# Kernel tuning notes

Measured on AMD Instinct MI355X. Metric: run time of the kernel, lower is better.

The kernel has to match this reference:

```python
import jax, jax.numpy as jnp
import numpy as np

V, E, H0, H1 = 32000, 512, 1024, 1024
B, S = 32, 128


def setup_inputs() -> dict:
    key = jax.random.key(0)
    ks = jax.random.split(key, 10)
    s = 0.02
    tokens = jax.random.randint(ks[0], (B, S), 0, V)
    emb = jax.random.normal(ks[1], (V, E), dtype=jnp.float32) * s
    W0 = jax.random.normal(ks[2], (E, H0), dtype=jnp.float32) * s
    U0 = jax.random.normal(ks[3], (H0, H0), dtype=jnp.float32) * s
    b0 = jnp.zeros((H0,), dtype=jnp.float32)
    W1 = jax.random.normal(ks[4], (H0, H1), dtype=jnp.float32) * s
    U1 = jax.random.normal(ks[5], (H1, H1), dtype=jnp.float32) * s
    b1 = jnp.zeros((H1,), dtype=jnp.float32)
    Wd = jax.random.normal(ks[6], (H1, V), dtype=jnp.float32) * s
    bd = jnp.zeros((V,), dtype=jnp.float32)
    return {"tokens": tokens, "emb": emb, "W0": W0, "U0": U0, "b0": b0,
            "W1": W1, "U1": U1, "b1": b1, "Wd": Wd, "bd": bd}


def reference(tokens, emb, W0, U0, b0, W1, U1, b1, Wd, bd):
    # Embedding lookup: [B, S, E]
    x = emb[tokens]
    # Stacked SimpleRNN: h_t = tanh(x W + h U + b), layer1 feeds layer2 per step.
    xt = jnp.swapaxes(x, 0, 1)  # [S, B, E] for scan over time

    def step(carry, x_t):
        h0, h1 = carry
        h0 = jnp.tanh(x_t @ W0 + h0 @ U0 + b0)
        h1 = jnp.tanh(h0 @ W1 + h1 @ U1 + b1)
        return (h0, h1), h1

    batch = tokens.shape[0]
    init = (jnp.zeros((batch, W0.shape[1]), dtype=x.dtype),
            jnp.zeros((batch, W1.shape[1]), dtype=x.dtype))
    _, ys = jax.lax.scan(step, init, xt)  # ys: [S, B, H1]
    ys = jnp.swapaxes(ys, 0, 1)  # [B, S, H1]
    # Final dense to vocab logits: [B, S, V]
    return ys @ Wd + bd
```

## Files before the change

### kernel.cpp

```cpp
#include <hip/hip_runtime.h>
#include <hip/hip_bf16.h>
#include <cstdint>

typedef __attribute__((ext_vector_type(8))) short bf16x8;
typedef __attribute__((ext_vector_type(4))) float f32x4;
typedef __attribute__((ext_vector_type(4))) unsigned int u32x4;

#define V_ 32000
#define E_ 512
#define H_ 1024
#define B_ 32
#define S_ 128

#define L1WG 16
#define L2WG 32
#define NWGS 48
#define NTILES 250
#define GWGS (16 * NTILES)

typedef __attribute__((address_space(1))) unsigned int* gas1_t;
typedef __attribute__((address_space(3))) unsigned int* las3_t;
__device__ __forceinline__ void load_lds16(const void* g, void* l) {
  __builtin_amdgcn_global_load_lds((gas1_t)g, (las3_t)l, 16, 0, 0);
}

__device__ __forceinline__ void ldx4_sc(u32x4* d, const void* p) {
  asm volatile("global_load_dwordx4 %0, %1, off sc0 sc1" : "=v"(*d) : "v"(p) : "memory");
}
__device__ __forceinline__ unsigned ld_sc(const unsigned* p) {
  unsigned d;
  asm volatile("global_load_dword %0, %1, off sc0 sc1\n\ts_waitcnt vmcnt(0)"
               : "=v"(d) : "v"(p) : "memory");
  return d;
}
__device__ __forceinline__ void st_swap(unsigned* p, unsigned v) {
  asm volatile("global_atomic_swap %0, %1, off sc1" :: "v"(p), "v"(v) : "memory");
}
__device__ __forceinline__ void st_swap2(uint2* p, uint2 v) {
  asm volatile("global_atomic_swap_x2 %0, %1, off sc1" :: "v"(p), "v"(v) : "memory");
}
#define WAITVM0()                                     \
  asm volatile("s_waitcnt vmcnt(0)" ::: "memory");    \
  __builtin_amdgcn_sched_barrier(0)

__device__ __forceinline__ unsigned short bfbits(float x) {
  __hip_bfloat16 b = __float2bfloat16(x);
  union { __hip_bfloat16 b; unsigned short u; } c;
  c.b = b;
  return c.u;
}

__device__ __forceinline__ uint2 pack_rows(const float f[4], int lane, int j) {
  uint2 v2[4];
#pragma unroll
  for (int r = 0; r < 4; ++r) {
    const float o = __shfl_xor(f[r], 1);
    const float lo = (lane & 1) ? o : f[r];
    const float hi = (lane & 1) ? f[r] : o;
    const unsigned pk = (unsigned)bfbits(lo) | ((unsigned)bfbits(hi) << 16);
    const unsigned q2 = __shfl_xor(pk, 2);
    v2[r].x = (j & 2) ? q2 : pk;
    v2[r].y = (j & 2) ? pk : q2;
  }
  const int rs = lane & 3;
  return rs == 0 ? v2[0] : rs == 1 ? v2[1] : rs == 2 ? v2[2] : v2[3];
}

__global__ __launch_bounds__(256) void transpose_f32_bf16(
    const float* __restrict__ src, __hip_bfloat16* __restrict__ dst, int R, int C) {
  __shared__ float tile[32][33];
  const int c0 = blockIdx.x << 5, r0 = blockIdx.y << 5;
  const int tx = threadIdx.x & 31, ty = threadIdx.x >> 5;
#pragma unroll
  for (int i = 0; i < 32; i += 8)
    tile[ty + i][tx] = src[(size_t)(r0 + ty + i) * C + (c0 + tx)];
  __syncthreads();
#pragma unroll
  for (int i = 0; i < 32; i += 8)
    dst[(size_t)(c0 + ty + i) * R + (r0 + tx)] = __float2bfloat16(tile[tx][ty + i]);
}

__global__ __launch_bounds__(256) void gather_embed(
    const int* __restrict__ tokens, const float* __restrict__ emb,
    __hip_bfloat16* __restrict__ Xg) {
  const int r = blockIdx.x;
  const int t = r >> 5, b = r & 31;
  const int tok = tokens[b * S_ + t];
  const float* e = emb + (size_t)tok * E_;
  __hip_bfloat16* o = Xg + (size_t)r * E_;
  for (int k = threadIdx.x; k < E_; k += 256) o[k] = __float2bfloat16(e[k]);
}

__global__ __launch_bounds__(256) void make_frag_w(
    const float* __restrict__ W, __hip_bfloat16* __restrict__ F) {
  const int idx = blockIdx.x * 256 + threadIdx.x;
  const int lane = idx & 63, kb = (idx >> 6) & 31, g = idx >> 11;
  const int j = (g << 4) + (lane & 15);
  const int kbase = (kb << 5) + ((lane >> 4) << 3);
  __hip_bfloat16* o = F + (size_t)idx * 8;
#pragma unroll
  for (int e = 0; e < 8; ++e) o[e] = __float2bfloat16(W[(size_t)(kbase + e) * H_ + j]);
}

__global__ __launch_bounds__(256) void gemm_bf16_tn(
    const __hip_bfloat16* __restrict__ A, const __hip_bfloat16* __restrict__ Bt,
    const float* __restrict__ bias, float* __restrict__ C, int M, int N, int K) {
  __shared__ __hip_bfloat16 ldsA[2][128 * 64];
  __shared__ __hip_bfloat16 ldsB[2][128 * 64];
  const int nwg = gridDim.x * gridDim.y;
  int L = blockIdx.y * gridDim.x + blockIdx.x;
  L = ((L & 7) * (nwg >> 3)) + (L >> 3);
  const int m0 = (L / gridDim.x) << 7;
  const int n0 = (L % gridDim.x) << 7;
  const int tid = threadIdx.x, wave = tid >> 6, lane = tid & 63;
  const int wr = wave >> 1, wc = wave & 1;
  f32x4 acc[4][4];
#pragma unroll
  for (int i = 0; i < 4; ++i)
#pragma unroll
    for (int jj = 0; jj < 4; ++jj) acc[i][jj] = (f32x4){0.f, 0.f, 0.f, 0.f};

  auto stage = [&](int buf, int k0) {
#pragma unroll
    for (int i = 0; i < 4; ++i) {
      const int c = i * 4 + wave;
      const int idx = (c << 6) + lane;
      const int row = idx >> 3, kk = (idx & 7) << 3;
      load_lds16(A + (size_t)(m0 + row) * K + (k0 + kk), &ldsA[buf][c * 512]);
      load_lds16(Bt + (size_t)(n0 + row) * K + (k0 + kk), &ldsB[buf][c * 512]);
    }
  };
  stage(0, 0);
  __syncthreads();
  int cur = 0;
  for (int k0 = 0; k0 < K; k0 += 64) {
    if (k0 + 64 < K) stage(cur ^ 1, k0 + 64);
    __builtin_amdgcn_s_setprio(1);
#pragma unroll
    for (int ks = 0; ks < 2; ++ks) {
      bf16x8 af[4], bfr[4];
#pragma unroll
      for (int mi = 0; mi < 4; ++mi)
        af[mi] = *(const bf16x8*)(&ldsA[cur][0] +
                                  (((wr << 6) + (mi << 4) + (lane & 15)) << 6) +
                                  (ks << 5) + ((lane >> 4) << 3));
#pragma unroll
      for (int ni = 0; ni < 4; ++ni)
        bfr[ni] = *(const bf16x8*)(&ldsB[cur][0] +
                                   (((wc << 6) + (ni << 4) + (lane & 15)) << 6) +
                                   (ks << 5) + ((lane >> 4) << 3));
#pragma unroll
      for (int mi = 0; mi < 4; ++mi)
#pragma unroll
        for (int ni = 0; ni < 4; ++ni)
          acc[mi][ni] =
              __builtin_amdgcn_mfma_f32_16x16x32_bf16(af[mi], bfr[ni], acc[mi][ni], 0, 0, 0);
    }
    __builtin_amdgcn_s_setprio(0);
    __syncthreads();
    cur ^= 1;
  }
#pragma unroll
  for (int mi = 0; mi < 4; ++mi) {
#pragma unroll
    for (int ni = 0; ni < 4; ++ni) {
      const int n = n0 + (wc << 6) + (ni << 4) + (lane & 15);
      const float bn = bias[n];
#pragma unroll
      for (int r = 0; r < 4; ++r) {
        const int m = m0 + (wr << 6) + (mi << 4) + ((lane >> 4) << 2) + r;
        C[(size_t)m * N + n] = acc[mi][ni][r] + bn;
      }
    }
  }
}

__global__ __launch_bounds__(512, 1) void rnn_vocab_fused(
    const __hip_bfloat16* __restrict__ U0f, const __hip_bfloat16* __restrict__ W1f,
    const __hip_bfloat16* __restrict__ U1f, const float* __restrict__ xw,
    const float* __restrict__ b1,
    __hip_bfloat16* __restrict__ h0buf,
    __hip_bfloat16* __restrict__ h1buf,
    __hip_bfloat16* __restrict__ Y,
    unsigned* __restrict__ flags,
    const __hip_bfloat16* __restrict__ Wdt,
    const float* __restrict__ bd, float* __restrict__ out) {
  __shared__ char smem[135168];
  const int tid = threadIdx.x, wave = tid >> 6, lane = tid & 63;

  if (blockIdx.x < NWGS) {
    char* sA0 = smem;
    char* sA1 = smem + 65536;
    float* pad = (float*)(smem + 131072);
    const int g = blockIdx.x;
    const bool isL1 = (g < L1WG);
    const int mi = wave & 1;
    const int cg = isL1 ? (wave >> 1) : ((wave >> 1) & 1);
    const int mat = isL1 ? 0 : (wave >> 2);
    const int colbase = isL1 ? (g << 6) : ((g - L1WG) << 5);
    const int j = colbase + (cg << 4) + (lane & 15);
    const int gg = (colbase >> 4) + cg;
    const int rowbase = (mi << 4) + ((lane >> 4) << 2);
    const int rs = lane & 3;
    const int ra = (mi << 4) + (lane & 15);
    const int q4 = (lane >> 4) << 4;
    const float b1j = b1[j];

    const __hip_bfloat16* wb = isL1 ? U0f : (mat == 0 ? W1f : U1f);
    bf16x8 wfr[32];
#pragma unroll
    for (int kb = 0; kb < 32; ++kb)
      wfr[kb] = *(const bf16x8*)(wb + (size_t)((((gg << 5) + kb) << 6) + lane) * 8);

    if (!isL1) {
      for (int i = tid; i < 4096; i += 512) *(uint4*)(sA1 + i * 16) = (uint4){0u, 0u, 0u, 0u};
    }
    __syncthreads();

    const int stg_row = tid >> 7;
    const int stg_colb = (tid & 127) << 4;
    const unsigned* fpoll = flags + ((lane < NWGS ? lane : NWGS - 1) << 4);

    if (isL1) {
      for (int p = 0; p < S_; ++p) {
        const float* xrow = xw + ((size_t)p << 15);
        float xv[4];
#pragma unroll
        for (int r = 0; r < 4; ++r) xv[r] = xrow[(rowbase + r) * H_ + j];
        if (p >= 1) {
          const unsigned tgt =
              (lane < L1WG) ? (unsigned)p : (p >= 3 ? (unsigned)(p - 3) : 0u);
          unsigned v;
          do { v = ld_sc(fpoll); } while (__any(v < tgt));
          const char* src0 = (const char*)(h0buf + ((size_t)((p - 1) & 3) << 15));
          u32x4 t0[8];
#pragma unroll
          for (int i = 0; i < 8; ++i) ldx4_sc(&t0[i], src0 + (size_t)(((i << 9) + tid) << 4));
          WAITVM0();
#pragma unroll
          for (int i = 0; i < 8; ++i) {
            const int row = stg_row + (i << 2);
            *(u32x4*)(sA0 + (row << 11) + (stg_colb ^ ((row & 7) << 4))) = t0[i];
          }
          __syncthreads();
        }
        f32x4 acc = {0.f, 0.f, 0.f, 0.f};
        if (p >= 1) {
#pragma unroll
          for (int kb = 0; kb < 32; ++kb) {
            bf16x8 a = *(const bf16x8*)(
                sA0 + (ra << 11) + ((((kb << 6) + q4)) ^ ((ra & 7) << 4)));
            acc = __builtin_amdgcn_mfma_f32_16x16x32_bf16(a, wfr[kb], acc, 0, 0, 0);
          }
        }
        float f[4];
#pragma unroll
        for (int r = 0; r < 4; ++r) f[r] = tanhf(acc[r] + xv[r]);
        uint2 vsel = pack_rows(f, lane, j);
        uint2* h4 = (uint2*)(h0buf + ((size_t)(p & 3) << 15));
        st_swap2(h4 + (rowbase + rs) * (H_ / 4) + (j >> 2), vsel);
        WAITVM0();
        __syncthreads();
        if (tid == 0) st_swap(flags + (g << 4), (unsigned)(p + 1));
      }
    } else {
      for (int t = 0; t < S_; ++t) {
        {
          const unsigned tgt = (lane < L1WG) ? (unsigned)(t + 1) : (unsigned)t;
          unsigned v;
          do { v = ld_sc(fpoll); } while (__any(v < tgt));
        }
        {
          const char* src0 = (const char*)(h0buf + ((size_t)(t & 3) << 15));
          u32x4 t0[8], t1[8];
#pragma unroll
          for (int i = 0; i < 8; ++i) ldx4_sc(&t0[i], src0 + (size_t)(((i << 9) + tid) << 4));
          if (t >= 1) {
            const char* src1 = (const char*)(h1buf + ((size_t)((t - 1) & 1) << 15));
#pragma unroll
            for (int i = 0; i < 8; ++i) ldx4_sc(&t1[i], src1 + (size_t)(((i << 9) + tid) << 4));
          }
          WAITVM0();
#pragma unroll
          for (int i = 0; i < 8; ++i) {
            const int row = stg_row + (i << 2);
            *(u32x4*)(sA0 + (row << 11) + (stg_colb ^ ((row & 7) << 4))) = t0[i];
          }
          if (t >= 1) {
#pragma unroll
            for (int i = 0; i < 8; ++i) {
              const int row = stg_row + (i << 2);
              *(u32x4*)(sA1 + (row << 11) + (stg_colb ^ ((row & 7) << 4))) = t1[i];
            }
          }
          __syncthreads();
        }
        const char* sA = (mat == 0) ? sA0 : sA1;
        f32x4 acc = {0.f, 0.f, 0.f, 0.f};
#pragma unroll
        for (int kb = 0; kb < 32; ++kb) {
          bf16x8 a = *(const bf16x8*)(
              sA + (ra << 11) + ((((kb << 6) + q4)) ^ ((ra & 7) << 4)));
          acc = __builtin_amdgcn_mfma_f32_16x16x32_bf16(a, wfr[kb], acc, 0, 0, 0);
        }
        const int pair = wave & 3;
        if (mat == 0) *(f32x4*)(pad + pair * 256 + lane * 4) = acc;
        __syncthreads();
        if (mat == 1) {
          f32x4 accW = *(const f32x4*)(pad + pair * 256 + lane * 4);
          float f[4];
#pragma unroll
          for (int r = 0; r < 4; ++r) f[r] = tanhf(acc[r] + accW[r] + b1j);
          uint2 vsel = pack_rows(f, lane, j);
          const int bb = rowbase + rs;
          uint2* h4 = (uint2*)(h1buf + ((size_t)(t & 1) << 15));
          st_swap2(h4 + bb * (H_ / 4) + (j >> 2), vsel);
          st_swap2((uint2*)Y + ((size_t)((t << 5) + bb)) * (H_ / 4) + (j >> 2), vsel);
        }
        WAITVM0();
        __syncthreads();
        if (tid == 0) st_swap(flags + (g << 4), (unsigned)(t + 1));
      }
    }
    return;
  }

  const int bid = blockIdx.x - NWGS;
  const int mt = bid / NTILES, nt = bid - mt * NTILES;
  const int m0 = mt << 8, n0 = nt << 7;
  {
    const unsigned tgt = (unsigned)((mt << 3) + 8);
    if (wave == 0) {
      const unsigned* fp = flags + ((L1WG + (lane & 31)) << 4);
      while (true) {
        unsigned v = ld_sc(fp);
        if (!__any(v < tgt)) break;
        asm volatile("s_sleep 8");
      }
    }
    __syncthreads();
  }
  __hip_bfloat16* ldsA = (__hip_bfloat16*)smem;
  __hip_bfloat16* ldsB = (__hip_bfloat16*)(smem + 65536);
  const int wr = wave >> 1, wc = wave & 1;
  f32x4 acc[4][4];
#pragma unroll
  for (int i = 0; i < 4; ++i)
#pragma unroll
    for (int jj = 0; jj < 4; ++jj) acc[i][jj] = (f32x4){0.f, 0.f, 0.f, 0.f};

  u32x4 ta[4];
  auto issueA = [&](int k0) {
#pragma unroll
    for (int i = 0; i < 4; ++i) {
      const int chunk = (i << 9) + tid;
      const int row = chunk >> 3, kk = (chunk & 7) << 3;
      ldx4_sc(&ta[i], Y + (size_t)(m0 + row) * H_ + k0 + kk);
    }
  };
  auto issueB = [&](int buf, int k0) {
#pragma unroll
    for (int i = 0; i < 2; ++i) {
      const int c = (i << 3) + wave;
      const int idx = (c << 6) + lane;
      const int row = idx >> 3, kk = (idx & 7) << 3;
      load_lds16(Wdt + (size_t)(n0 + row) * H_ + k0 + kk, ldsB + buf * 8192 + c * 512);
    }
  };
  auto writeA = [&](int buf) {
#pragma unroll
    for (int i = 0; i < 4; ++i) {
      const int chunk = (i << 9) + tid;
      *(u32x4*)((char*)ldsA + buf * 32768 + chunk * 16) = ta[i];
    }
  };

  issueA(0);
  issueB(0, 0);
  WAITVM0();
  writeA(0);
  __syncthreads();
  int cur = 0;
  for (int k0 = 0; k0 < H_; k0 += 64) {
    const bool more = (k0 + 64 < H_);
    if (more) {
      issueA(k0 + 64);
      issueB(cur ^ 1, k0 + 64);
    }
    __builtin_amdgcn_s_setprio(1);
#pragma unroll
    for (int ks = 0; ks < 2; ++ks) {
      bf16x8 af[4], bfr[4];
#pragma unroll
      for (int mi = 0; mi < 4; ++mi)
        af[mi] = *(const bf16x8*)(ldsA + cur * 16384 +
                                  (((wr << 6) + (mi << 4) + (lane & 15)) << 6) +
                                  (ks << 5) + ((lane >> 4) << 3));
#pragma unroll
      for (int ni = 0; ni < 4; ++ni)
        bfr[ni] = *(const bf16x8*)(ldsB + cur * 8192 +
                                   (((ni << 4) + (lane & 15)) << 6) +
                                   (ks << 5) + ((lane >> 4) << 3) + (wc << 12));
#pragma unroll
      for (int mi = 0; mi < 4; ++mi)
#pragma unroll
        for (int ni = 0; ni < 4; ++ni)
          acc[mi][ni] =
              __builtin_amdgcn_mfma_f32_16x16x32_bf16(af[mi], bfr[ni], acc[mi][ni], 0, 0, 0);
    }
    __builtin_amdgcn_s_setprio(0);
    if (more) {
      WAITVM0();
      writeA(cur ^ 1);
    }
    __syncthreads();
    cur ^= 1;
  }
#pragma unroll
  for (int mi = 0; mi < 4; ++mi) {
#pragma unroll
    for (int ni = 0; ni < 4; ++ni) {
      const int n = n0 + (wc << 6) + (ni << 4) + (lane & 15);
      const float bn = bd[n];
#pragma unroll
      for (int r = 0; r < 4; ++r) {
        const int m = m0 + (wr << 6) + (mi << 4) + ((lane >> 4) << 2) + r;
        const size_t orow = (size_t)(m & 31) * S_ + (m >> 5);
        out[orow * V_ + n] = acc[mi][ni][r] + bn;
      }
    }
  }
}

extern "C" void kernel_launch(void* const* d_in, const int* in_sizes, int n_in, void* d_out,
                              int out_size, void* d_ws, size_t ws_size, hipStream_t stream) {
  const int* tokens = (const int*)d_in[0];
  const float* emb = (const float*)d_in[1];
  const float* W0 = (const float*)d_in[2];
  const float* U0 = (const float*)d_in[3];
  const float* b0 = (const float*)d_in[4];
  const float* W1 = (const float*)d_in[5];
  const float* U1 = (const float*)d_in[6];
  const float* b1 = (const float*)d_in[7];
  const float* Wd = (const float*)d_in[8];
  const float* bd = (const float*)d_in[9];
  float* out = (float*)d_out;

  char* ws = (char*)d_ws;
  __hip_bfloat16* Wdt = (__hip_bfloat16*)ws;  ws += (size_t)V_ * H_ * 2;
  __hip_bfloat16* W0t = (__hip_bfloat16*)ws;  ws += (size_t)H_ * E_ * 2;
  __hip_bfloat16* Xg = (__hip_bfloat16*)ws;   ws += (size_t)4096 * E_ * 2;
  __hip_bfloat16* U0f = (__hip_bfloat16*)ws;  ws += (size_t)H_ * H_ * 2;
  __hip_bfloat16* W1f = (__hip_bfloat16*)ws;  ws += (size_t)H_ * H_ * 2;
  __hip_bfloat16* U1f = (__hip_bfloat16*)ws;  ws += (size_t)H_ * H_ * 2;
  float* xw = (float*)ws;                     ws += (size_t)4096 * H_ * 4;
  __hip_bfloat16* h0buf = (__hip_bfloat16*)ws; ws += 4 * B_ * H_ * 2;
  __hip_bfloat16* h1buf = (__hip_bfloat16*)ws; ws += 2 * B_ * H_ * 2;
  __hip_bfloat16* Y = (__hip_bfloat16*)ws;    ws += (size_t)4096 * H_ * 2;
  unsigned* flags = (unsigned*)ws;            ws += 4096;

  transpose_f32_bf16<<<dim3(V_ / 32, H_ / 32), 256, 0, stream>>>(Wd, Wdt, H_, V_);
  transpose_f32_bf16<<<dim3(H_ / 32, E_ / 32), 256, 0, stream>>>(W0, W0t, E_, H_);
  gather_embed<<<4096, 256, 0, stream>>>(tokens, emb, Xg);
  make_frag_w<<<512, 256, 0, stream>>>(U0, U0f);
  make_frag_w<<<512, 256, 0, stream>>>(W1, W1f);
  make_frag_w<<<512, 256, 0, stream>>>(U1, U1f);
  hipMemsetAsync(flags, 0, 4096, stream);

  gemm_bf16_tn<<<dim3(H_ / 128, 4096 / 128), 256, 0, stream>>>(Xg, W0t, b0, xw, 4096, H_, E_);

  rnn_vocab_fused<<<NWGS + GWGS, 512, 0, stream>>>(U0f, W1f, U1f, xw, b1, h0buf, h1buf, Y,
                                                   flags, Wdt, bd, out);
}
```

Before: 1.077 ms.

## Store Y and Wd in MFMA fragment order and stage both via direct LDS loads

The RNN now writes its hidden outputs Y in a pre-fragmented MFMA-operand layout, and Wd is converted by make_frag_w into the same fragment layout instead of being transposed. The vocab GEMM tiles can then load both operands with global_load_lds straight into LDS. This drops the register round trip and the wait-then-write step for the A tile, and the LDS reads become contiguous per lane. In exchange, the RNN's Y stores are more scattered, and the Wd conversion kernel reads columns with a strided pattern.

```diff
diff --git a/kernel.cpp b/kernel.cpp
--- a/kernel.cpp
+++ b/kernel.cpp
@@ -92,14 +92,14 @@
 }
 
 __global__ __launch_bounds__(256) void make_frag_w(
-    const float* __restrict__ W, __hip_bfloat16* __restrict__ F) {
+    const float* __restrict__ W, __hip_bfloat16* __restrict__ F, int ncols) {
   const int idx = blockIdx.x * 256 + threadIdx.x;
   const int lane = idx & 63, kb = (idx >> 6) & 31, g = idx >> 11;
   const int j = (g << 4) + (lane & 15);
   const int kbase = (kb << 5) + ((lane >> 4) << 3);
   __hip_bfloat16* o = F + (size_t)idx * 8;
 #pragma unroll
-  for (int e = 0; e < 8; ++e) o[e] = __float2bfloat16(W[(size_t)(kbase + e) * H_ + j]);
+  for (int e = 0; e < 8; ++e) o[e] = __float2bfloat16(W[(size_t)(kbase + e) * ncols + j]);
 }
 
 __global__ __launch_bounds__(256) void gemm_bf16_tn(
@@ -181,9 +181,9 @@
     const float* __restrict__ b1,
     __hip_bfloat16* __restrict__ h0buf,
     __hip_bfloat16* __restrict__ h1buf,
-    __hip_bfloat16* __restrict__ Y,
+    __hip_bfloat16* __restrict__ Yf,
     unsigned* __restrict__ flags,
-    const __hip_bfloat16* __restrict__ Wdt,
+    const __hip_bfloat16* __restrict__ Wdf,
     const float* __restrict__ bd, float* __restrict__ out) {
   __shared__ char smem[135168];
   const int tid = threadIdx.x, wave = tid >> 6, lane = tid & 63;
@@ -315,7 +315,11 @@
           const int bb = rowbase + rs;
           uint2* h4 = (uint2*)(h1buf + ((size_t)(t & 1) << 15));
           st_swap2(h4 + bb * (H_ / 4) + (j >> 2), vsel);
-          st_swap2((uint2*)Y + ((size_t)((t << 5) + bb)) * (H_ / 4) + (j >> 2), vsel);
+          const int jb = j & ~3;
+          const size_t fo =
+              (((size_t)((t << 1) + (bb >> 4)) << 5) + (jb >> 5)) * 64 +
+              (((jb >> 3) & 3) << 4) + (bb & 15);
+          st_swap2((uint2*)((char*)Yf + fo * 16 + ((jb & 7) << 1)), vsel);
         }
         WAITVM0();
         __syncthreads();
@@ -340,8 +344,6 @@
     }
     __syncthreads();
   }
-  __hip_bfloat16* ldsA = (__hip_bfloat16*)smem;
-  __hip_bfloat16* ldsB = (__hip_bfloat16*)(smem + 65536);
   const int wr = wave >> 1, wc = wave & 1;
   f32x4 acc[4][4];
 #pragma unroll
@@ -349,43 +351,37 @@
 #pragma unroll
     for (int jj = 0; jj < 4; ++jj) acc[i][jj] = (f32x4){0.f, 0.f, 0.f, 0.f};
 
-  u32x4 ta[4];
-  auto issueA = [&](int k0) {
+  const char* Yc = (const char*)Yf;
+  const char* Wc = (const char*)Wdf;
+  auto stageA = [&](int buf, int k0) {
 #pragma unroll
     for (int i = 0; i < 4; ++i) {
-      const int chunk = (i << 9) + tid;
-      const int row = chunk >> 3, kk = (chunk & 7) << 3;
-      ldx4_sc(&ta[i], Y + (size_t)(m0 + row) * H_ + k0 + kk);
+      const int c = (i << 3) + wave;
+      const int mg = c >> 1, kb = c & 1;
+      const char* src = Yc + ((((size_t)(m0 >> 4) + mg) << 5) + (k0 >> 5) + kb) * 1024 +
+                        (lane << 4);
+      load_lds16(src, smem + buf * 32768 + c * 1024);
     }
   };
-  auto issueB = [&](int buf, int k0) {
+  auto stageB = [&](int buf, int k0) {
 #pragma unroll
     for (int i = 0; i < 2; ++i) {
       const int c = (i << 3) + wave;
-      const int idx = (c << 6) + lane;
-      const int row = idx >> 3, kk = (idx & 7) << 3;
-      load_lds16(Wdt + (size_t)(n0 + row) * H_ + k0 + kk, ldsB + buf * 8192 + c * 512);
+      const int ng = c >> 1, kb = c & 1;
+      const char* src = Wc + ((((size_t)(n0 >> 4) + ng) << 5) + (k0 >> 5) + kb) * 1024 +
+                        (lane << 4);
+      load_lds16(src, smem + 65536 + buf * 16384 + c * 1024);
     }
   };
-  auto writeA = [&](int buf) {
-#pragma unroll
-    for (int i = 0; i < 4; ++i) {
-      const int chunk = (i << 9) + tid;
-      *(u32x4*)((char*)ldsA + buf * 32768 + chunk * 16) = ta[i];
-    }
-  };
-
-  issueA(0);
-  issueB(0, 0);
-  WAITVM0();
-  writeA(0);
+
+  stageA(0, 0);
+  stageB(0, 0);
   __syncthreads();
   int cur = 0;
   for (int k0 = 0; k0 < H_; k0 += 64) {
-    const bool more = (k0 + 64 < H_);
-    if (more) {
-      issueA(k0 + 64);
-      issueB(cur ^ 1, k0 + 64);
+    if (k0 + 64 < H_) {
+      stageA(cur ^ 1, k0 + 64);
+      stageB(cur ^ 1, k0 + 64);
     }
     __builtin_amdgcn_s_setprio(1);
 #pragma unroll
@@ -393,14 +389,12 @@
       bf16x8 af[4], bfr[4];
 #pragma unroll
       for (int mi = 0; mi < 4; ++mi)
-        af[mi] = *(const bf16x8*)(ldsA + cur * 16384 +
-                                  (((wr << 6) + (mi << 4) + (lane & 15)) << 6) +
-                                  (ks << 5) + ((lane >> 4) << 3));
+        af[mi] = *(const bf16x8*)(smem + cur * 32768 +
+                                  ((((wr << 2) + mi) << 1) + ks) * 1024 + (lane << 4));
 #pragma unroll
       for (int ni = 0; ni < 4; ++ni)
-        bfr[ni] = *(const bf16x8*)(ldsB + cur * 8192 +
-                                   (((ni << 4) + (lane & 15)) << 6) +
-                                   (ks << 5) + ((lane >> 4) << 3) + (wc << 12));
+        bfr[ni] = *(const bf16x8*)(smem + 65536 + cur * 16384 +
+                                   ((((wc << 2) + ni) << 1) + ks) * 1024 + (lane << 4));
 #pragma unroll
       for (int mi = 0; mi < 4; ++mi)
 #pragma unroll
@@ -409,10 +403,6 @@
               __builtin_amdgcn_mfma_f32_16x16x32_bf16(af[mi], bfr[ni], acc[mi][ni], 0, 0, 0);
     }
     __builtin_amdgcn_s_setprio(0);
-    if (more) {
-      WAITVM0();
-      writeA(cur ^ 1);
-    }
     __syncthreads();
     cur ^= 1;
   }
@@ -447,7 +437,7 @@
   float* out = (float*)d_out;
 
   char* ws = (char*)d_ws;
-  __hip_bfloat16* Wdt = (__hip_bfloat16*)ws;  ws += (size_t)V_ * H_ * 2;
+  __hip_bfloat16* Wdf = (__hip_bfloat16*)ws;  ws += (size_t)V_ * H_ * 2;
   __hip_bfloat16* W0t = (__hip_bfloat16*)ws;  ws += (size_t)H_ * E_ * 2;
   __hip_bfloat16* Xg = (__hip_bfloat16*)ws;   ws += (size_t)4096 * E_ * 2;
   __hip_bfloat16* U0f = (__hip_bfloat16*)ws;  ws += (size_t)H_ * H_ * 2;
@@ -456,19 +446,19 @@
   float* xw = (float*)ws;                     ws += (size_t)4096 * H_ * 4;
   __hip_bfloat16* h0buf = (__hip_bfloat16*)ws; ws += 4 * B_ * H_ * 2;
   __hip_bfloat16* h1buf = (__hip_bfloat16*)ws; ws += 2 * B_ * H_ * 2;
-  __hip_bfloat16* Y = (__hip_bfloat16*)ws;    ws += (size_t)4096 * H_ * 2;
+  __hip_bfloat16* Yf = (__hip_bfloat16*)ws;   ws += (size_t)4096 * H_ * 2;
   unsigned* flags = (unsigned*)ws;            ws += 4096;
 
-  transpose_f32_bf16<<<dim3(V_ / 32, H_ / 32), 256, 0, stream>>>(Wd, Wdt, H_, V_);
   transpose_f32_bf16<<<dim3(H_ / 32, E_ / 32), 256, 0, stream>>>(W0, W0t, E_, H_);
   gather_embed<<<4096, 256, 0, stream>>>(tokens, emb, Xg);
-  make_frag_w<<<512, 256, 0, stream>>>(U0, U0f);
-  make_frag_w<<<512, 256, 0, stream>>>(W1, W1f);
-  make_frag_w<<<512, 256, 0, stream>>>(U1, U1f);
+  make_frag_w<<<512, 256, 0, stream>>>(U0, U0f, H_);
+  make_frag_w<<<512, 256, 0, stream>>>(W1, W1f, H_);
+  make_frag_w<<<512, 256, 0, stream>>>(U1, U1f, H_);
+  make_frag_w<<<16000, 256, 0, stream>>>(Wd, Wdf, V_);
   hipMemsetAsync(flags, 0, 4096, stream);
 
   gemm_bf16_tn<<<dim3(H_ / 128, 4096 / 128), 256, 0, stream>>>(Xg, W0t, b0, xw, 4096, H_, E_);
 
-  rnn_vocab_fused<<<NWGS + GWGS, 512, 0, stream>>>(U0f, W1f, U1f, xw, b1, h0buf, h1buf, Y,
-                                                   flags, Wdt, bd, out);
-}
+  rnn_vocab_fused<<<NWGS + GWGS, 512, 0, stream>>>(U0f, W1f, U1f, xw, b1, h0buf, h1buf, Yf,
+                                                   flags, Wdf, bd, out);
+}
```

Result: no change. 1.084 ms (+0.7%).
